# Kernel tuning notes

Hardware: AMD Instinct MI355X
Metric: run time of the kernel (lower is better)

## Reference

```python
import jax, jax.numpy as jnp
import numpy as np

B, S, D, H = 64, 256, 2048, 16
HD = D // H

def setup_inputs() -> dict:
    key = jax.random.key(0)
    k1, k2, k3 = jax.random.split(key, 3)
    x = jax.random.normal(k1, (B, S, D), dtype=jnp.float32)
    # torch Linear weights: [out_features, in_features], scaled like kaiming-ish init
    w_qkv = jax.random.normal(k2, (3 * D, D), dtype=jnp.float32) * (1.0 / np.sqrt(D))
    w_o = jax.random.normal(k3, (D, D), dtype=jnp.float32) * (1.0 / np.sqrt(D))
    return {"x": x, "w_qkv": w_qkv, "w_o": w_o}

def reference(x, w_qkv, w_o):
    b, s, d = x.shape
    qkv = jnp.einsum('bsd,ed->bse', x, w_qkv)            # [B,S,3D]
    qkv = qkv.reshape(b, s, 3, H, HD).transpose(2, 0, 3, 1, 4)  # [3,B,H,S,HD]
    q, k, v = qkv[0], qkv[1], qkv[2]
    scores = jnp.einsum('bhqd,bhkd->bhqk', q, k) * (HD ** -0.5)  # [B,H,S,S]
    causal = jnp.triu(jnp.ones((s, s), dtype=bool), 1)
    scores = jnp.where(causal, jnp.float32(-1e9), scores)
    a = jax.nn.softmax(scores, axis=-1)
    ctx = jnp.einsum('bhqk,bhkd->bhqd', a, v)            # [B,H,S,HD]
    ctx = ctx.transpose(0, 2, 1, 3).reshape(b, s, d)     # [B,S,D]
    return jnp.einsum('bsd,ed->bse', ctx, w_o)
```

## Files before the change

### kernel.cpp

```cpp
#include <hip/hip_runtime.h>

#define NB 64
#define NS 256
#define ND 2048
#define NH 16
#define NHD 128

typedef unsigned short ushort_t;
typedef __attribute__((ext_vector_type(8))) __bf16 bf16x8;
typedef __attribute__((ext_vector_type(4))) short shortx4;
typedef __attribute__((ext_vector_type(4))) float f32x4;
typedef __attribute__((ext_vector_type(4))) unsigned short ushortx4;

__device__ __forceinline__ unsigned short f2bf(float f) {
  union { float f; unsigned int u; } v; v.f = f;
  unsigned int r = v.u + 0x7FFFu + ((v.u >> 16) & 1u);
  return (unsigned short)(r >> 16);
}

__device__ __forceinline__ void gload16(const void* g, void* l) {
  __builtin_amdgcn_global_load_lds(
      (__attribute__((address_space(1))) void*)(void*)(g),
      (__attribute__((address_space(3))) void*)(l), 16, 0, 0);
}

__device__ __forceinline__ unsigned lds_off(const void* p) {
  return (unsigned)(size_t)(__attribute__((address_space(3))) const void*)p;
}

template<int OFF>
__device__ __forceinline__ shortx4 tr16(unsigned addr) {
  shortx4 d;
  asm volatile("ds_read_b64_tr_b16 %0, %1 offset:%2"
               : "=v"(d) : "v"(addr), "i"(OFF));
  return d;
}

__global__ void cast3_f32_bf16(const float* __restrict__ x, const float* __restrict__ wq,
                               const float* __restrict__ wo, ushort_t* __restrict__ xb,
                               ushort_t* __restrict__ wqb, ushort_t* __restrict__ wob) {
  long bi = blockIdx.x;
  const float* src; ushort_t* dst;
  if (bi < 32768) { src = x; dst = xb; }
  else if (bi < 32768 + 12288) { bi -= 32768; src = wq; dst = wqb; }
  else { bi -= 32768 + 12288; src = wo; dst = wob; }
  const long i = (bi * 256 + threadIdx.x) * 4;
  float4 v = *reinterpret_cast<const float4*>(src + i);
  ushortx4 o;
  o.x = f2bf(v.x); o.y = f2bf(v.y); o.z = f2bf(v.z); o.w = f2bf(v.w);
  *reinterpret_cast<ushortx4*>(dst + i) = o;
}

template<int MODE>
__global__ __launch_bounds__(512, 2) void gemm256(const ushort_t* __restrict__ A,
                                                  const ushort_t* __restrict__ Bt,
                                                  float* __restrict__ Cf,
                                                  ushort_t* __restrict__ Cq,
                                                  int M, int N, int K) {
  extern __shared__ char smem[];
  const int tid = threadIdx.x;
  const int wv = tid >> 6, lane = tid & 63;
  const int l15 = lane & 15, lg = lane >> 4;
  const int wm = wv >> 2, wn = wv & 3;

  const int nbn = N >> 8;
  const int nwg = (M >> 8) * nbn;
  const int bid = blockIdx.x;
  const int q8 = nwg >> 3, r8 = nwg & 7;
  const int xcd = bid & 7, lin = bid >> 3;
  const int wg = (xcd < r8 ? xcd * (q8 + 1) : r8 * (q8 + 1) + (xcd - r8) * q8) + lin;
  const int m0 = (wg / nbn) << 8;
  const int n0 = (wg % nbn) << 8;

  const int srow = tid >> 3;
  const int sce = ((tid & 7) * 8) ^ ((srow & 7) << 3);
  const ushort_t* pa = A  + (long)(m0 + srow) * K + sce;
  const ushort_t* pb = Bt + (long)(n0 + srow) * K + sce;

  const int cx = (l15 & 7) << 4;
  const int c0 = (lg * 16) ^ cx;
  const int c1 = (64 + lg * 16) ^ cx;

  f32x4 acc[8][4] = {};
  const int nkt = K >> 6;

  #pragma unroll
  for (int ch = 0; ch < 4; ++ch) {
    gload16(pa + (long)(ch * 64) * K, smem + ch * 8192 + wv * 1024);
    gload16(pb + (long)(ch * 64) * K, smem + 32768 + ch * 8192 + wv * 1024);
  }
  asm volatile("s_waitcnt vmcnt(0)" ::: "memory");
  __builtin_amdgcn_s_barrier();

  for (int t = 0; t < nkt; ++t) {
    const char* rb = smem + (t & 1) * 65536;
    const long kof = (long)t * 64;
    if (t + 1 < nkt) {
      char* db = smem + ((t + 1) & 1) * 65536 + wv * 1024;
      #pragma unroll
      for (int ch = 0; ch < 4; ++ch) {
        gload16(pa + (long)(ch * 64) * K + kof + 64, db + ch * 8192);
        gload16(pb + (long)(ch * 64) * K + kof + 64, db + 32768 + ch * 8192);
      }
    }
    bf16x8 af[8][2], bf[4][2];
    #pragma unroll
    for (int i = 0; i < 8; ++i) {
      const char* base = rb + (wm * 128 + i * 16 + l15) * 128;
      af[i][0] = *reinterpret_cast<const bf16x8*>(base + c0);
      af[i][1] = *reinterpret_cast<const bf16x8*>(base + c1);
    }
    #pragma unroll
    for (int j = 0; j < 4; ++j) {
      const char* base = rb + 32768 + (wn * 64 + j * 16 + l15) * 128;
      bf[j][0] = *reinterpret_cast<const bf16x8*>(base + c0);
      bf[j][1] = *reinterpret_cast<const bf16x8*>(base + c1);
    }
    asm volatile("s_waitcnt lgkmcnt(0)" ::: "memory");
    __builtin_amdgcn_sched_barrier(0);
    __builtin_amdgcn_s_setprio(1);
    #pragma unroll
    for (int kk = 0; kk < 2; ++kk)
      #pragma unroll
      for (int i = 0; i < 8; ++i)
        #pragma unroll
        for (int j = 0; j < 4; ++j)
          acc[i][j] = __builtin_amdgcn_mfma_f32_16x16x32_bf16(af[i][kk], bf[j][kk], acc[i][j], 0, 0, 0);
    __builtin_amdgcn_s_setprio(0);
    __builtin_amdgcn_sched_barrier(0);
    asm volatile("s_waitcnt vmcnt(0)" ::: "memory");
    __builtin_amdgcn_s_barrier();
  }

  #pragma unroll
  for (int k = 0; k < 8; ++k) {
    const int mrow = m0 + wm * 128 + k * 16 + lg * 4;
    #pragma unroll
    for (int j = 0; j < 4; ++j) {
      const int n = n0 + wn * 64 + j * 16 + l15;
      #pragma unroll
      for (int r = 0; r < 4; ++r) {
        const int m = mrow + r;
        const float v = acc[k][j][r];
        if (MODE == 0) {
          Cf[(long)m * N + n] = v;
        } else {
          const int tq = n >> 11, hh = (n >> 7) & 15, hd = n & 127;
          const int b = m >> 8, s = m & 255;
          Cq[((((long)tq * NB + b) * NH + hh) * NS + s) * NHD + hd] = f2bf(v);
        }
      }
    }
  }
}

__global__ __launch_bounds__(512, 2) void attn_fused(const ushort_t* __restrict__ qkv,
                                                     ushort_t* __restrict__ ctx) {
  __shared__ char vsm[32768];
  const int bh = blockIdx.x;
  const int b = bh >> 4, h = bh & 15;
  const int tid = threadIdx.x;
  const int wave = tid >> 6, lane = tid & 63;
  const int l15 = lane & 15, lg = lane >> 4;
  const long head_off = ((long)(b * NH + h)) * (NS * NHD);
  const ushort_t* Qp = qkv + head_off;
  const ushort_t* Kp = qkv + (long)NB * NH * NS * NHD + head_off;
  const ushort_t* Vp = qkv + 2L * NB * NH * NS * NHD + head_off;
  const int q0 = wave * 32;
  const int klast = (q0 + 31) >> 6;

  const int t7 = tid & 127;
  const int srowv = ((t7 >> 3) << 2) | ((t7 >> 1) & 3);
  const int vcol = (tid >> 7) * 16 + (t7 & 1) * 8;
  const ushort_t* vsrc = Vp + srowv * NHD + vcol;

  bf16x8 qf[2][4];
  #pragma unroll
  for (int ni = 0; ni < 2; ++ni)
    #pragma unroll
    for (int kk = 0; kk < 4; ++kk)
      qf[ni][kk] = *reinterpret_cast<const bf16x8*>(Qp + (q0 + ni * 16 + l15) * NHD + kk * 32 + lg * 8);

  f32x4 o[8][2] = {};
  float mstate[2] = {-1e30f, -1e30f};
  float lstate[2] = {0.f, 0.f};
  const float scale = 0.08838834764831845f;

  gload16(vsrc, vsm + wave * 1024);
  gload16(vsrc + 64, vsm + 8192 + wave * 1024);
  asm volatile("s_waitcnt vmcnt(0)" ::: "memory");
  __builtin_amdgcn_s_barrier();

  for (int kt = 0; kt < 4; ++kt) {
    if (kt + 1 < 4) {
      char* db = vsm + ((kt + 1) & 1) * 16384 + wave * 1024;
      const ushort_t* s = vsrc + (kt + 1) * 64 * NHD;
      gload16(s, db);
      gload16(s + 64, db + 8192);
    }
    shortx4 p[4][2];
    const bool act = (kt <= klast);
    if (act) {
      f32x4 st[4][2] = {};
      #pragma unroll
      for (int kk = 0; kk < 4; ++kk) {
        bf16x8 kf[4];
        #pragma unroll
        for (int mi = 0; mi < 4; ++mi)
          kf[mi] = *reinterpret_cast<const bf16x8*>(Kp + (kt * 64 + mi * 16 + l15) * NHD + kk * 32 + lg * 8);
        #pragma unroll
        for (int mi = 0; mi < 4; ++mi)
          #pragma unroll
          for (int ni = 0; ni < 2; ++ni)
            st[mi][ni] = __builtin_amdgcn_mfma_f32_16x16x32_bf16(kf[mi], qf[ni][kk], st[mi][ni], 0, 0, 0);
      }
      const bool dom = (kt == klast);
      #pragma unroll
      for (int mi = 0; mi < 4; ++mi)
        #pragma unroll
        for (int ni = 0; ni < 2; ++ni)
          #pragma unroll
          for (int r = 0; r < 4; ++r) {
            const int kc = kt * 64 + mi * 16 + lg * 4 + r;
            const int q = q0 + ni * 16 + l15;
            float v = st[mi][ni][r] * scale;
            if (dom && kc > q) v = -1e30f;
            st[mi][ni][r] = v;
          }
      #pragma unroll
      for (int ni = 0; ni < 2; ++ni) {
        float tmax = -1e30f;
        #pragma unroll
        for (int mi = 0; mi < 4; ++mi)
          #pragma unroll
          for (int r = 0; r < 4; ++r) tmax = fmaxf(tmax, st[mi][ni][r]);
        tmax = fmaxf(tmax, __shfl_xor(tmax, 16, 64));
        tmax = fmaxf(tmax, __shfl_xor(tmax, 32, 64));
        const float mnew = fmaxf(mstate[ni], tmax);
        const float alpha = __expf(mstate[ni] - mnew);
        float tsum = 0.f;
        #pragma unroll
        for (int mi = 0; mi < 4; ++mi)
          #pragma unroll
          for (int r = 0; r < 4; ++r) {
            const float pe = __expf(st[mi][ni][r] - mnew);
            st[mi][ni][r] = pe;
            tsum += pe;
          }
        tsum += __shfl_xor(tsum, 16, 64);
        tsum += __shfl_xor(tsum, 32, 64);
        lstate[ni] = lstate[ni] * alpha + tsum;
        mstate[ni] = mnew;
        #pragma unroll
        for (int f = 0; f < 8; ++f)
          #pragma unroll
          for (int r = 0; r < 4; ++r) o[f][ni][r] *= alpha;
        #pragma unroll
        for (int mi = 0; mi < 4; ++mi)
          #pragma unroll
          for (int r = 0; r < 4; ++r) p[mi][ni][r] = (short)f2bf(st[mi][ni][r]);
      }
      const unsigned va = lds_off(vsm) + (unsigned)((kt & 1) * 16384 + lane * 8);
#define PVF(F)                                                                  \
      {                                                                         \
        shortx4 v0 = tr16<(F)*2048 +    0>(va);                                 \
        shortx4 v1 = tr16<(F)*2048 +  512>(va);                                 \
        shortx4 v2 = tr16<(F)*2048 + 1024>(va);                                 \
        shortx4 v3 = tr16<(F)*2048 + 1536>(va);                                 \
        asm volatile("s_waitcnt lgkmcnt(0)" ::: "memory");                      \
        __builtin_amdgcn_sched_barrier(0);                                      \
        o[F][0] = __builtin_amdgcn_mfma_f32_16x16x16bf16_1k(v0, p[0][0], o[F][0], 0, 0, 0); \
        o[F][1] = __builtin_amdgcn_mfma_f32_16x16x16bf16_1k(v0, p[0][1], o[F][1], 0, 0, 0); \
        o[F][0] = __builtin_amdgcn_mfma_f32_16x16x16bf16_1k(v1, p[1][0], o[F][0], 0, 0, 0); \
        o[F][1] = __builtin_amdgcn_mfma_f32_16x16x16bf16_1k(v1, p[1][1], o[F][1], 0, 0, 0); \
        o[F][0] = __builtin_amdgcn_mfma_f32_16x16x16bf16_1k(v2, p[2][0], o[F][0], 0, 0, 0); \
        o[F][1] = __builtin_amdgcn_mfma_f32_16x16x16bf16_1k(v2, p[2][1], o[F][1], 0, 0, 0); \
        o[F][0] = __builtin_amdgcn_mfma_f32_16x16x16bf16_1k(v3, p[3][0], o[F][0], 0, 0, 0); \
        o[F][1] = __builtin_amdgcn_mfma_f32_16x16x16bf16_1k(v3, p[3][1], o[F][1], 0, 0, 0); \
      }
      PVF(0) PVF(1) PVF(2) PVF(3) PVF(4) PVF(5) PVF(6) PVF(7)
#undef PVF
    }
    asm volatile("s_waitcnt vmcnt(0)" ::: "memory");
    __builtin_amdgcn_s_barrier();
  }

  const float inv0 = 1.f / lstate[0], inv1 = 1.f / lstate[1];
  #pragma unroll
  for (int f = 0; f < 8; ++f)
    #pragma unroll
    for (int ni = 0; ni < 2; ++ni) {
      const float inv = ni ? inv1 : inv0;
      const int q = q0 + ni * 16 + l15;
      const int hd = f * 16 + lg * 4;
      ushortx4 ov;
      #pragma unroll
      for (int r = 0; r < 4; ++r) ov[r] = f2bf(o[f][ni][r] * inv);
      *reinterpret_cast<ushortx4*>(ctx + ((long)(b * NS + q)) * ND + h * NHD + hd) = ov;
    }
}

extern "C" void kernel_launch(void* const* d_in, const int* in_sizes, int n_in,
                              void* d_out, int out_size, void* d_ws, size_t ws_size,
                              hipStream_t stream) {
  const float* x     = (const float*)d_in[0];
  const float* w_qkv = (const float*)d_in[1];
  const float* w_o   = (const float*)d_in[2];
  char* ws = (char*)d_ws;
  if (ws_size < 369098752UL) return;
  ushort_t* xb    = (ushort_t*)(ws);
  ushort_t* wqkvb = (ushort_t*)(ws + 67108864L);
  ushort_t* wob   = (ushort_t*)(ws + 92274688L);
  ushort_t* qkvb  = (ushort_t*)(ws + 100663296L);
  ushort_t* ctxb  = (ushort_t*)(ws + 301989888L);

  cast3_f32_bf16<<<dim3(49152), 256, 0, stream>>>(x, w_qkv, w_o, xb, wqkvb, wob);

  const int lds_bytes = 2 * 65536;
  (void)hipFuncSetAttribute(reinterpret_cast<const void*>(&gemm256<1>),
                            hipFuncAttributeMaxDynamicSharedMemorySize, lds_bytes);
  (void)hipFuncSetAttribute(reinterpret_cast<const void*>(&gemm256<0>),
                            hipFuncAttributeMaxDynamicSharedMemorySize, lds_bytes);

  gemm256<1><<<dim3(64 * 24), 512, lds_bytes, stream>>>(xb, wqkvb, nullptr, qkvb,
                                                        NB * NS, 3 * ND, ND);
  attn_fused<<<dim3(NB * NH), 512, 0, stream>>>(qkvb, ctxb);
  gemm256<0><<<dim3(64 * 8), 512, lds_bytes, stream>>>(ctxb, wob, (float*)d_out, nullptr,
                                                       NB * NS, ND, ND);
}
```

Measured before the change: 674.7 us.

## Restructure GEMM main loop into quadrant-interleaved 8-wave pingpong pipeline

Replaces the simple double-buffered K loop in the bf16 GEMM with a schedule that processes two K tiles per iteration. Each tile is split into four MFMA quadrants, and the LDS reads and global-to-LDS stages for half-tiles are interleaved between them with barriers and partial vmcnt waits. The aim is to overlap LDS reads and global loads with MFMA work more finely and to cut register pressure by holding half of the A fragments at a time. In exchange it adds many more barriers per iteration, and its correctness depends on the buffer reuse ordering being right (for example, tile tO's B stage is deferred when it>0).

```diff
diff --git a/kernel.cpp b/kernel.cpp
--- a/kernel.cpp
+++ b/kernel.cpp
@@ -83,54 +83,88 @@
 
   f32x4 acc[8][4] = {};
   const int nkt = K >> 6;
-
-  #pragma unroll
-  for (int ch = 0; ch < 4; ++ch) {
-    gload16(pa + (long)(ch * 64) * K, smem + ch * 8192 + wv * 1024);
-    gload16(pb + (long)(ch * 64) * K, smem + 32768 + ch * 8192 + wv * 1024);
-  }
+  const int nit = nkt >> 1;
+
+#define STAGE_A(T_, H_)                                                        \
+  { char* d_ = smem + ((T_) & 1) * 65536 + (H_) * 16384 + wv * 1024;           \
+    gload16(pa + (long)((H_) * 128) * K + (long)(T_) * 64, d_);                \
+    gload16(pa + (long)((H_) * 128 + 64) * K + (long)(T_) * 64, d_ + 8192); }
+#define STAGE_B(T_, H_)                                                        \
+  { char* d_ = smem + ((T_) & 1) * 65536 + 32768 + (H_) * 16384 + wv * 1024;   \
+    gload16(pb + (long)((H_) * 128) * K + (long)(T_) * 64, d_);                \
+    gload16(pb + (long)((H_) * 128 + 64) * K + (long)(T_) * 64, d_ + 8192); }
+
+  STAGE_A(0, 0) STAGE_A(0, 1) STAGE_B(0, 0) STAGE_B(0, 1)
+  STAGE_A(1, 0) STAGE_A(1, 1) STAGE_B(1, 0) STAGE_B(1, 1)
   asm volatile("s_waitcnt vmcnt(0)" ::: "memory");
   __builtin_amdgcn_s_barrier();
 
-  for (int t = 0; t < nkt; ++t) {
-    const char* rb = smem + (t & 1) * 65536;
-    const long kof = (long)t * 64;
-    if (t + 1 < nkt) {
-      char* db = smem + ((t + 1) & 1) * 65536 + wv * 1024;
-      #pragma unroll
-      for (int ch = 0; ch < 4; ++ch) {
-        gload16(pa + (long)(ch * 64) * K + kof + 64, db + ch * 8192);
-        gload16(pb + (long)(ch * 64) * K + kof + 64, db + 32768 + ch * 8192);
-      }
-    }
-    bf16x8 af[8][2], bf[4][2];
-    #pragma unroll
-    for (int i = 0; i < 8; ++i) {
-      const char* base = rb + (wm * 128 + i * 16 + l15) * 128;
-      af[i][0] = *reinterpret_cast<const bf16x8*>(base + c0);
-      af[i][1] = *reinterpret_cast<const bf16x8*>(base + c1);
-    }
-    #pragma unroll
-    for (int j = 0; j < 4; ++j) {
-      const char* base = rb + 32768 + (wn * 64 + j * 16 + l15) * 128;
-      bf[j][0] = *reinterpret_cast<const bf16x8*>(base + c0);
-      bf[j][1] = *reinterpret_cast<const bf16x8*>(base + c1);
-    }
-    asm volatile("s_waitcnt lgkmcnt(0)" ::: "memory");
-    __builtin_amdgcn_sched_barrier(0);
-    __builtin_amdgcn_s_setprio(1);
-    #pragma unroll
-    for (int kk = 0; kk < 2; ++kk)
-      #pragma unroll
-      for (int i = 0; i < 8; ++i)
-        #pragma unroll
-        for (int j = 0; j < 4; ++j)
-          acc[i][j] = __builtin_amdgcn_mfma_f32_16x16x32_bf16(af[i][kk], bf[j][kk], acc[i][j], 0, 0, 0);
-    __builtin_amdgcn_s_setprio(0);
-    __builtin_amdgcn_sched_barrier(0);
-    asm volatile("s_waitcnt vmcnt(0)" ::: "memory");
-    __builtin_amdgcn_s_barrier();
-  }
+  bf16x8 a[4][2], a2[4][2], b[4][2];
+  const char* rbE = smem;
+  const char* rbO = smem + 65536;
+
+#define RD_A(DST_, RB_, ROFF_)                                                 \
+  _Pragma("unroll")                                                            \
+  for (int i_ = 0; i_ < 4; ++i_) {                                             \
+    const char* base_ = (RB_) + (wm * 128 + (ROFF_) + i_ * 16 + l15) * 128;    \
+    DST_[i_][0] = *reinterpret_cast<const bf16x8*>(base_ + c0);                \
+    DST_[i_][1] = *reinterpret_cast<const bf16x8*>(base_ + c1);                \
+  }
+#define RD_B(RB_, J0_)                                                         \
+  _Pragma("unroll")                                                            \
+  for (int j_ = 0; j_ < 2; ++j_) {                                             \
+    const char* base_ = (RB_) + 32768 + (wn * 64 + ((J0_) + j_) * 16 + l15) * 128; \
+    b[(J0_) + j_][0] = *reinterpret_cast<const bf16x8*>(base_ + c0);           \
+    b[(J0_) + j_][1] = *reinterpret_cast<const bf16x8*>(base_ + c1);           \
+  }
+#define QUANT(AI_, ARR_, J0_)                                                  \
+  __builtin_amdgcn_s_setprio(1);                                               \
+  _Pragma("unroll")                                                            \
+  for (int kk_ = 0; kk_ < 2; ++kk_)                                            \
+    _Pragma("unroll")                                                          \
+    for (int i_ = 0; i_ < 4; ++i_)                                             \
+      _Pragma("unroll")                                                        \
+      for (int j_ = 0; j_ < 2; ++j_)                                           \
+        acc[(AI_) + i_][(J0_) + j_] = __builtin_amdgcn_mfma_f32_16x16x32_bf16( \
+            ARR_[i_][kk_], b[(J0_) + j_][kk_], acc[(AI_) + i_][(J0_) + j_], 0, 0, 0); \
+  __builtin_amdgcn_s_setprio(0);
+#define LGKM0 asm volatile("s_waitcnt lgkmcnt(0)" ::: "memory");               \
+              __builtin_amdgcn_sched_barrier(0);
+#define VM4   asm volatile("s_waitcnt vmcnt(4)" ::: "memory");                 \
+              __builtin_amdgcn_sched_barrier(0);
+#define BAR   __builtin_amdgcn_s_barrier();
+
+  for (int it = 0; it < nit; ++it) {
+    const int tE = 2 * it, tO = tE + 1;
+    RD_A(a, rbE, 0) RD_B(rbE, 0)
+    if (it > 0) STAGE_B(tO, 0)
+    BAR LGKM0 QUANT(0, a, 0) BAR
+    RD_A(a2, rbE, 64) RD_B(rbE, 2)
+    if (it > 0) STAGE_B(tO, 1)
+    BAR LGKM0 QUANT(0, a, 2) BAR
+    if (tE + 2 < nkt) STAGE_A(tE + 2, 0)
+    BAR QUANT(4, a2, 0) BAR
+    if (tE + 2 < nkt) STAGE_A(tE + 2, 1)
+    BAR QUANT(4, a2, 2) VM4 BAR
+    RD_A(a, rbO, 0) RD_B(rbO, 0)
+    if (tE + 2 < nkt) STAGE_B(tE + 2, 0)
+    BAR LGKM0 QUANT(0, a, 0) BAR
+    RD_A(a2, rbO, 64) RD_B(rbO, 2)
+    if (tE + 2 < nkt) STAGE_B(tE + 2, 1)
+    BAR LGKM0 QUANT(0, a, 2) BAR
+    if (tO + 2 < nkt) STAGE_A(tO + 2, 0)
+    BAR QUANT(4, a2, 0) BAR
+    if (tO + 2 < nkt) STAGE_A(tO + 2, 1)
+    BAR QUANT(4, a2, 2) VM4 BAR
+  }
+#undef STAGE_A
+#undef STAGE_B
+#undef RD_A
+#undef RD_B
+#undef QUANT
+#undef LGKM0
+#undef VM4
+#undef BAR
 
   #pragma unroll
   for (int k = 0; k < 8; ++k) {
@@ -146,8 +180,8 @@
           Cf[(long)m * N + n] = v;
         } else {
           const int tq = n >> 11, hh = (n >> 7) & 15, hd = n & 127;
-          const int b = m >> 8, s = m & 255;
-          Cq[((((long)tq * NB + b) * NH + hh) * NS + s) * NHD + hd] = f2bf(v);
+          const int b_ = m >> 8, s = m & 255;
+          Cq[((((long)tq * NB + b_) * NH + hh) * NS + s) * NHD + hd] = f2bf(v);
         }
       }
     }
```

Measured after the change: 1.148 ms. +70.1%, slower.

## Restructure GEMM mainloop into 4-stage K=32 pipeline with split A/B staging

Applied to the files above, without the earlier changes.

Reworks the 256x256 GEMM mainloop from a double-buffered K=64 loop into a 4-slot ring of K=32 tiles, prefetching three tiles ahead. A and B loads are issued in separate halves, with an interleaved LDS layout (two rows packed per 128B line) and a new XOR swizzle. Fragment reads for the next tile are overlapped with MFMA on the current half. The aim is to hide global and LDS latency behind matrix math. In exchange the schedule relies on fine-grained vmcnt/lgkmcnt counts and extra barriers, which must stay correct.

```diff
diff --git a/kernel.cpp b/kernel.cpp
--- a/kernel.cpp
+++ b/kernel.cpp
@@ -72,65 +72,103 @@
   const int m0 = (wg / nbn) << 8;
   const int n0 = (wg % nbn) << 8;
 
-  const int srow = tid >> 3;
-  const int sce = ((tid & 7) * 8) ^ ((srow & 7) << 3);
-  const ushort_t* pa = A  + (long)(m0 + srow) * K + sce;
-  const ushort_t* pb = Bt + (long)(n0 + srow) * K + sce;
-
-  const int cx = (l15 & 7) << 4;
-  const int c0 = (lg * 16) ^ cx;
-  const int c1 = (64 + lg * 16) ^ cx;
+  const int ss = tid >> 3, sq = tid & 7;
+  const int su = sq ^ (ss & 7);
+  const int srow = 2 * ss + (su >> 2);
+  const int skel = (su & 3) * 8;
+  const ushort_t* pa = A  + (long)(m0 + srow) * K + skel;
+  const ushort_t* pb = Bt + (long)(n0 + srow) * K + skel;
+  const long c128 = (long)128 * K;
+
+  const int swz = (((l15 & 1) << 2) | lg) ^ ((l15 >> 1) & 7);
+  const int aoff = (wm * 64 + (l15 >> 1)) * 128 + swz * 16;
+  const int boff = 16384 + (wn * 32 + (l15 >> 1)) * 128 + swz * 16;
 
   f32x4 acc[8][4] = {};
-  const int nkt = K >> 6;
-
-  #pragma unroll
-  for (int ch = 0; ch < 4; ++ch) {
-    gload16(pa + (long)(ch * 64) * K, smem + ch * 8192 + wv * 1024);
-    gload16(pb + (long)(ch * 64) * K, smem + 32768 + ch * 8192 + wv * 1024);
-  }
+  const int nkt = K >> 5;
+
+#define STAGE_A(T_)                                                            \
+  { char* d_ = smem + ((T_) & 3) * 32768 + wv * 1024;                          \
+    gload16(pa + (long)(T_) * 32, d_);                                         \
+    gload16(pa + c128 + (long)(T_) * 32, d_ + 8192); }
+#define STAGE_B(T_)                                                            \
+  { char* d_ = smem + ((T_) & 3) * 32768 + 16384 + wv * 1024;                  \
+    gload16(pb + (long)(T_) * 32, d_);                                         \
+    gload16(pb + c128 + (long)(T_) * 32, d_ + 8192); }
+
+  STAGE_A(0) STAGE_B(0) STAGE_A(1) STAGE_B(1) STAGE_A(2) STAGE_B(2)
   asm volatile("s_waitcnt vmcnt(0)" ::: "memory");
   __builtin_amdgcn_s_barrier();
 
-  for (int t = 0; t < nkt; ++t) {
-    const char* rb = smem + (t & 1) * 65536;
-    const long kof = (long)t * 64;
-    if (t + 1 < nkt) {
-      char* db = smem + ((t + 1) & 1) * 65536 + wv * 1024;
-      #pragma unroll
-      for (int ch = 0; ch < 4; ++ch) {
-        gload16(pa + (long)(ch * 64) * K + kof + 64, db + ch * 8192);
-        gload16(pb + (long)(ch * 64) * K + kof + 64, db + 32768 + ch * 8192);
-      }
-    }
-    bf16x8 af[8][2], bf[4][2];
-    #pragma unroll
-    for (int i = 0; i < 8; ++i) {
-      const char* base = rb + (wm * 128 + i * 16 + l15) * 128;
-      af[i][0] = *reinterpret_cast<const bf16x8*>(base + c0);
-      af[i][1] = *reinterpret_cast<const bf16x8*>(base + c1);
-    }
-    #pragma unroll
-    for (int j = 0; j < 4; ++j) {
-      const char* base = rb + 32768 + (wn * 64 + j * 16 + l15) * 128;
-      bf[j][0] = *reinterpret_cast<const bf16x8*>(base + c0);
-      bf[j][1] = *reinterpret_cast<const bf16x8*>(base + c1);
-    }
-    asm volatile("s_waitcnt lgkmcnt(0)" ::: "memory");
-    __builtin_amdgcn_sched_barrier(0);
-    __builtin_amdgcn_s_setprio(1);
-    #pragma unroll
-    for (int kk = 0; kk < 2; ++kk)
-      #pragma unroll
-      for (int i = 0; i < 8; ++i)
-        #pragma unroll
-        for (int j = 0; j < 4; ++j)
-          acc[i][j] = __builtin_amdgcn_mfma_f32_16x16x32_bf16(af[i][kk], bf[j][kk], acc[i][j], 0, 0, 0);
-    __builtin_amdgcn_s_setprio(0);
-    __builtin_amdgcn_sched_barrier(0);
-    asm volatile("s_waitcnt vmcnt(0)" ::: "memory");
-    __builtin_amdgcn_s_barrier();
+  bf16x8 fA[4], fB[4], gA[4], gB[4];
+  #pragma unroll
+  for (int i = 0; i < 4; ++i)
+    fA[i] = *reinterpret_cast<const bf16x8*>(smem + aoff + i * 1024);
+  #pragma unroll
+  for (int j = 0; j < 4; ++j)
+    fB[j] = *reinterpret_cast<const bf16x8*>(smem + boff + j * 1024);
+
+#define TILE(T_, CA_, CB_, NA_, NB_)                                           \
+  {                                                                            \
+    const int t_ = (T_);                                                       \
+    const char* rb_ = smem + (t_ & 3) * 32768;                                 \
+                                                            \
+    bf16x8 ah1[4];                                                             \
+    _Pragma("unroll")                                                          \
+    for (int i_ = 0; i_ < 4; ++i_)                                             \
+      ah1[i_] = *reinterpret_cast<const bf16x8*>(rb_ + aoff + (4 + i_) * 1024);\
+    if (t_ + 3 < nkt) STAGE_A(t_ + 3)                                          \
+    __builtin_amdgcn_sched_barrier(0);                                         \
+    __builtin_amdgcn_s_barrier();                                              \
+    asm volatile("s_waitcnt lgkmcnt(4)" ::: "memory");                         \
+    __builtin_amdgcn_sched_barrier(0);                                         \
+    __builtin_amdgcn_s_setprio(1);                                             \
+    _Pragma("unroll")                                                          \
+    for (int i_ = 0; i_ < 4; ++i_)                                             \
+      _Pragma("unroll")                                                        \
+      for (int j_ = 0; j_ < 4; ++j_)                                           \
+        acc[i_][j_] = __builtin_amdgcn_mfma_f32_16x16x32_bf16(                 \
+            CA_[i_], CB_[j_], acc[i_][j_], 0, 0, 0);                           \
+    __builtin_amdgcn_s_setprio(0);                                             \
+    __builtin_amdgcn_sched_barrier(0);                                         \
+    if (t_ + 3 < nkt) asm volatile("s_waitcnt vmcnt(6)" ::: "memory");         \
+    else              asm volatile("s_waitcnt vmcnt(0)" ::: "memory");         \
+    __builtin_amdgcn_sched_barrier(0);                                         \
+    __builtin_amdgcn_s_barrier();                                              \
+                                                            \
+    if (t_ + 1 < nkt) {                                                        \
+      const char* rn_ = smem + ((t_ + 1) & 3) * 32768;                         \
+      _Pragma("unroll")                                                        \
+      for (int i_ = 0; i_ < 4; ++i_)                                           \
+        NA_[i_] = *reinterpret_cast<const bf16x8*>(rn_ + aoff + i_ * 1024);    \
+      _Pragma("unroll")                                                        \
+      for (int j_ = 0; j_ < 4; ++j_)                                           \
+        NB_[j_] = *reinterpret_cast<const bf16x8*>(rn_ + boff + j_ * 1024);    \
+    }                                                                          \
+    if (t_ + 3 < nkt) STAGE_B(t_ + 3)                                          \
+    __builtin_amdgcn_sched_barrier(0);                                         \
+    __builtin_amdgcn_s_barrier();                                              \
+    if (t_ + 1 < nkt) asm volatile("s_waitcnt lgkmcnt(8)" ::: "memory");       \
+    else              asm volatile("s_waitcnt lgkmcnt(0)" ::: "memory");       \
+    __builtin_amdgcn_sched_barrier(0);                                         \
+    __builtin_amdgcn_s_setprio(1);                                             \
+    _Pragma("unroll")                                                          \
+    for (int i_ = 0; i_ < 4; ++i_)                                             \
+      _Pragma("unroll")                                                        \
+      for (int j_ = 0; j_ < 4; ++j_)                                           \
+        acc[4 + i_][j_] = __builtin_amdgcn_mfma_f32_16x16x32_bf16(             \
+            ah1[i_], CB_[j_], acc[4 + i_][j_], 0, 0, 0);                       \
+    __builtin_amdgcn_s_setprio(0);                                             \
+    __builtin_amdgcn_s_barrier();                                              \
   }
+
+  for (int t = 0; t < nkt; t += 2) {
+    TILE(t,     fA, fB, gA, gB)
+    TILE(t + 1, gA, gB, fA, fB)
+  }
+#undef TILE
+#undef STAGE_A
+#undef STAGE_B
 
   #pragma unroll
   for (int k = 0; k < 8; ++k) {
@@ -146,8 +184,8 @@
           Cf[(long)m * N + n] = v;
         } else {
           const int tq = n >> 11, hh = (n >> 7) & 15, hd = n & 127;
-          const int b = m >> 8, s = m & 255;
-          Cq[((((long)tq * NB + b) * NH + hh) * NS + s) * NHD + hd] = f2bf(v);
+          const int b_ = m >> 8, s = m & 255;
+          Cq[((((long)tq * NB + b_) * NH + hh) * NS + s) * NHD + hd] = f2bf(v);
         }
       }
     }
@@ -316,7 +354,7 @@
 
   cast3_f32_bf16<<<dim3(49152), 256, 0, stream>>>(x, w_qkv, w_o, xb, wqkvb, wob);
 
-  const int lds_bytes = 2 * 65536;
+  const int lds_bytes = 4 * 32768;
   (void)hipFuncSetAttribute(reinterpret_cast<const void*>(&gemm256<1>),
                             hipFuncAttributeMaxDynamicSharedMemorySize, lds_bytes);
   (void)hipFuncSetAttribute(reinterpret_cast<const void*>(&gemm256<0>),
```

After: 715.9 us. 1.06x slower.
